# Kernel optimization log

Hardware: AMD Instinct MI355X
Metric: run time of the kernel (lower is better)

Reference implementation:

```python
import jax, jax.numpy as jnp
import numpy as np

N = 4096      # num_nodes (unbatched seq len for the transformer)
D = 128       # input_dim = window = d_model
H = 4         # num_heads
DH = D // H
DFF = 2048    # PyTorch TransformerEncoderLayer default dim_feedforward
HID = 256     # hidden_dim
OUT = 64      # output_dim
E = 131072    # num_edges (avg degree 32)
EPS = 1e-5    # LayerNorm eps (torch default)


def layer_norm(x, g, b):
    mu = jnp.mean(x, axis=-1, keepdims=True)
    var = jnp.var(x, axis=-1, keepdims=True)
    return (x - mu) * jax.lax.rsqrt(var + EPS) * g + b


def gcn_conv(x, W, b, src, dst):
    # PyG GCNConv: h = x W^T; add self-loops; symmetric deg^-1/2 norm; scatter-add at dst; + bias
    h = x @ W.T
    loop = jnp.arange(N)
    s = jnp.concatenate([src, loop])
    t = jnp.concatenate([dst, loop])
    deg = jax.ops.segment_sum(jnp.ones_like(t, dtype=h.dtype), t, num_segments=N)
    dinv = jnp.where(deg > 0, jax.lax.rsqrt(jnp.maximum(deg, 1e-12)), 0.0)
    norm = dinv[s] * dinv[t]                                   # [E+N]
    out = jax.ops.segment_sum(h[s] * norm[:, None], t, num_segments=N)
    return out + b


def setup_inputs() -> dict:
    key = jax.random.key(0)
    ks = jax.random.split(key, 12)
    sc = 0.05
    w = lambda k, shape: jax.random.normal(k, shape, dtype=jnp.float32) * sc
    return {
        "x": jax.random.normal(ks[0], (N, D), dtype=jnp.float32),
        "edge_index": jax.random.randint(ks[1], (2, E), 0, N),
        "in_proj_w": w(ks[2], (3 * D, D)),
        "in_proj_b": jnp.zeros((3 * D,), jnp.float32),
        "out_proj_w": w(ks[3], (D, D)),
        "out_proj_b": jnp.zeros((D,), jnp.float32),
        "ln1_g": jnp.ones((D,), jnp.float32),
        "ln1_b": jnp.zeros((D,), jnp.float32),
        "ffn_w1": w(ks[4], (DFF, D)),
        "ffn_b1": jnp.zeros((DFF,), jnp.float32),
        "ffn_w2": w(ks[5], (D, DFF)),
        "ffn_b2": jnp.zeros((D,), jnp.float32),
        "ln2_g": jnp.ones((D,), jnp.float32),
        "ln2_b": jnp.zeros((D,), jnp.float32),
        "gcn1_w": w(ks[6], (HID, D)),
        "gcn1_b": jnp.zeros((HID,), jnp.float32),
        "gcn2_w": w(ks[7], (HID, HID)),
        "gcn2_b": jnp.zeros((HID,), jnp.float32),
        "gcn3_w": w(ks[8], (OUT, HID)),
        "gcn3_b": jnp.zeros((OUT,), jnp.float32),
    }


def reference(x, edge_index, in_proj_w, in_proj_b, out_proj_w, out_proj_b,
              ln1_g, ln1_b, ffn_w1, ffn_b1, ffn_w2, ffn_b2, ln2_g, ln2_b,
              gcn1_w, gcn1_b, gcn2_w, gcn2_b, gcn3_w, gcn3_b):
    src, dst = edge_index[0], edge_index[1]
    # --- TransformerEncoderLayer (post-norm, relu, dropout=0, unbatched [N, D]) ---
    qkv = x @ in_proj_w.T + in_proj_b
    q, k, v = jnp.split(qkv, 3, axis=-1)
    q = q.reshape(N, H, DH)
    k = k.reshape(N, H, DH)
    v = v.reshape(N, H, DH)
    scores = jnp.einsum('nhd,mhd->hnm', q, k) / jnp.sqrt(jnp.float32(DH))
    attn = jax.nn.softmax(scores, axis=-1)
    ctx = jnp.einsum('hnm,mhd->nhd', attn, v).reshape(N, D)
    attn_out = ctx @ out_proj_w.T + out_proj_b
    y = layer_norm(x + attn_out, ln1_g, ln1_b)
    ff = jax.nn.relu(y @ ffn_w1.T + ffn_b1) @ ffn_w2.T + ffn_b2
    z = layer_norm(y + ff, ln2_g, ln2_b)
    # x.squeeze(-1) is a no-op since window (=128) > 1
    # --- 3-layer GCN with ReLU between layers ---
    h = jax.nn.relu(gcn_conv(z, gcn1_w, gcn1_b, src, dst))
    h = jax.nn.relu(gcn_conv(h, gcn2_w, gcn2_b, src, dst))
    return gcn_conv(h, gcn3_w, gcn3_b, src, dst)
```

## Files before the change

### kernel.cpp

```cpp
#include <hip/hip_runtime.h>


typedef unsigned short u16;
typedef __attribute__((ext_vector_type(8))) short bf16x8;
typedef __attribute__((ext_vector_type(4))) float f32x4;

__device__ __forceinline__ float b2f(u16 u) {
  union { unsigned int i; float f; } x; x.i = ((unsigned int)u) << 16; return x.f;
}
__device__ __forceinline__ u16 f2b(float f) {
  union { float f; unsigned int i; } x; x.f = f;
  unsigned int r = x.i + 0x7FFFu + ((x.i >> 16) & 1u);
  return (u16)(r >> 16);
}
__device__ __forceinline__ float ld1(const void* p, size_t i, int bf) {
  return bf ? b2f(((const u16*)p)[i]) : ((const float*)p)[i];
}

__device__ void gemm_body(
    int bx, int by, int bz, int nz,
    const void* __restrict__ A, const void* __restrict__ B,
    const void* __restrict__ bias, void* __restrict__ C, void* __restrict__ C2,
    int N, int K, int lda, int ldb, int bRow0, int bK0, int flags,
    const int* __restrict__ dflag, const float* __restrict__ divL)
{
  const int wbf = *dflag;
  const int abf = (flags & 64) ? 0 : ((flags & 16) ? wbf : 1);
  __shared__ u16 As[64][128];
  __shared__ u16 Bs[64][128];
  const int tid = threadIdx.x;
  const int wv = tid >> 6, l = tid & 63;
  const int lr = l & 15, lq = l >> 4;
  const int row0 = by * 64, col0 = bx * 64;
  const int qr = 32 * (wv >> 1), qc = 32 * (wv & 1);
  const int sr = tid >> 2, sb = tid & 3;
  const int Kz = K / nz;
  const int k0 = bz * Kz;
  f32x4 acc[2][2] = {};
  for (int kt = k0; kt < k0 + Kz; kt += 128) {
    __syncthreads();
#pragma unroll
    for (int g = 0; g < 4; g++) {
      int b = sb + 4 * g;
      int cc = b * 8;
      int bs = (b ^ (sr & 15)) * 8;
      size_t offA = (size_t)(row0 + sr) * lda + kt + cc;
      if (abf) {
        *(bf16x8*)&As[sr][bs] = *(const bf16x8*)((const u16*)A + offA);
      } else {
        const float* pf = (const float*)A + offA;
        float iv = divL
            ? 1.0f / divL[(size_t)((kt + cc) >> 5) * 4096 + row0 + sr]
            : 1.0f;
        float4 f0 = *(const float4*)pf, f1 = *(const float4*)(pf + 4);
        u16 t[8] = {f2b(f0.x*iv), f2b(f0.y*iv), f2b(f0.z*iv), f2b(f0.w*iv),
                    f2b(f1.x*iv), f2b(f1.y*iv), f2b(f1.z*iv), f2b(f1.w*iv)};
        *(bf16x8*)&As[sr][bs] = *(bf16x8*)t;
      }
      size_t offB = (size_t)(bRow0 + col0 + sr) * ldb + bK0 + kt + cc;
      if (wbf) {
        *(bf16x8*)&Bs[sr][bs] = *(const bf16x8*)((const u16*)B + offB);
      } else {
        const float* pf = (const float*)B + offB;
        float4 f0 = *(const float4*)pf, f1 = *(const float4*)(pf + 4);
        u16 t[8] = {f2b(f0.x), f2b(f0.y), f2b(f0.z), f2b(f0.w),
                    f2b(f1.x), f2b(f1.y), f2b(f1.z), f2b(f1.w)};
        *(bf16x8*)&Bs[sr][bs] = *(bf16x8*)t;
      }
    }
    __syncthreads();
#pragma unroll
    for (int kk = 0; kk < 4; kk++) {
      int bxs = ((4 * kk + lq) ^ lr) * 8;
      bf16x8 a0 = *(const bf16x8*)&As[qr + lr][bxs];
      bf16x8 a1 = *(const bf16x8*)&As[qr + 16 + lr][bxs];
      bf16x8 b0 = *(const bf16x8*)&Bs[qc + lr][bxs];
      bf16x8 b1 = *(const bf16x8*)&Bs[qc + 16 + lr][bxs];
      acc[0][0] = __builtin_amdgcn_mfma_f32_16x16x32_bf16(a0, b0, acc[0][0], 0, 0, 0);
      acc[0][1] = __builtin_amdgcn_mfma_f32_16x16x32_bf16(a0, b1, acc[0][1], 0, 0, 0);
      acc[1][0] = __builtin_amdgcn_mfma_f32_16x16x32_bf16(a1, b0, acc[1][0], 0, 0, 0);
      acc[1][1] = __builtin_amdgcn_mfma_f32_16x16x32_bf16(a1, b1, acc[1][1], 0, 0, 0);
    }
  }
  if ((flags & 128) && col0 >= 256) {
#pragma unroll
    for (int i = 0; i < 2; i++) {
#pragma unroll
      for (int j = 0; j < 2; j++) {
        int colg = col0 + qc + 16 * j + lr;
        int d = colg - 256;
        int rowbase = row0 + qr + 16 * i + lq * 4;
        float bb = ld1(bias, colg, wbf);
        ushort4 pv = make_ushort4(
            f2b(acc[i][j][0] + bb), f2b(acc[i][j][1] + bb),
            f2b(acc[i][j][2] + bb), f2b(acc[i][j][3] + bb));
        *(ushort4*)((u16*)C2 + (size_t)d * 4096 + rowbase) = pv;
      }
    }
    return;
  }
  const int ldc = (flags & 128) ? 256 : N;
#pragma unroll
  for (int i = 0; i < 2; i++) {
#pragma unroll
    for (int j = 0; j < 2; j++) {
#pragma unroll
      for (int r = 0; r < 4; r++) {
        int row = row0 + qr + 16 * i + lq * 4 + r;
        int col = col0 + qc + 16 * j + lr;
        float v = acc[i][j][r];
        if (flags & 8) v += ld1(bias, bRow0 + col, wbf);
        if (flags & 1) v = fmaxf(v, 0.f);
        size_t idx = (size_t)row * ldc + col;
        if (flags & 32) {
          ((float*)C)[(size_t)bz * 524288 + idx] = v;
        } else if (flags & 4) {
          float* Cf = (float*)C;
          if (flags & 2) v += Cf[idx];
          Cf[idx] = v;
        } else {
          ((u16*)C)[idx] = f2b(v);
        }
      }
    }
  }
}

__global__ __launch_bounds__(256) void gemm_mfma(
    const void* __restrict__ A, const void* __restrict__ B,
    const void* __restrict__ bias, void* __restrict__ C, void* __restrict__ C2,
    int N, int K, int lda, int ldb, int bRow0, int bK0, int flags,
    const int* __restrict__ dflag, const float* __restrict__ divL)
{
  gemm_body(blockIdx.x, blockIdx.y, blockIdx.z, gridDim.z,
            A, B, bias, C, C2, N, K, lda, ldb, bRow0, bK0, flags, dflag, divL);
}

__global__ __launch_bounds__(256) void det_zero(
    const void* __restrict__ x, int* __restrict__ flag,
    int* __restrict__ cursor)
{
  if (blockIdx.x == 0) {
    __shared__ int cnt;
    if (threadIdx.x == 0) cnt = 0;
    __syncthreads();
    const u16* p = (const u16*)x;
    int c = 0;
    for (int i = threadIdx.x; i < 4096; i += 256) {
      int e = (p[i] >> 7) & 0xFF;
      if (e >= 140) c++;
    }
    atomicAdd(&cnt, c);
    __syncthreads();
    if (threadIdx.x == 0) flag[0] = (cnt < 64) ? 1 : 0;
  } else {
    cursor[(blockIdx.x - 1) * 256 + threadIdx.x] = 0;
  }
}

__global__ __launch_bounds__(256) void csr_inproj(
    const void* __restrict__ xin, const void* __restrict__ W,
    const void* __restrict__ bias, void* __restrict__ qkQK, void* __restrict__ Vg,
    const int* __restrict__ dflag,
    const int* __restrict__ src, const int* __restrict__ dst,
    int* __restrict__ cursor, int* __restrict__ csr, int E)
{
  if (blockIdx.x < 384) {
    gemm_body(blockIdx.x % 6, blockIdx.x / 6, 0, 1,
              xin, W, bias, qkQK, Vg, 384, 128, 128, 128, 0, 0,
               8 | 16 | 128, dflag, nullptr);
  } else {
    int e = (blockIdx.x - 384) * 256 + threadIdx.x;
    if (e < E) {
      int t = dst[e];
      int pos = atomicAdd(&cursor[t], 1);
      if (pos < 128) csr[(t << 7) + pos] = src[e];
    }
  }
}

__global__ __launch_bounds__(256) void attn_part(
    const u16* __restrict__ qk, const u16* __restrict__ Vg,
    float* __restrict__ O, float* __restrict__ L)
{
  const int qt = blockIdx.x, h = blockIdx.y, kc = blockIdx.z;
  const int n0 = qt * 64;
  __shared__ u16 Qs[64][32];
  __shared__ u16 Ks[128][32];
  __shared__ u16 Vt[32][128];
  __shared__ u16 Ps[64][128];
  const int tid = threadIdx.x;
  const int wv = tid >> 6, l = tid & 63;
  const int lr = l & 15, lq = l >> 4;
  const int sr = tid >> 2, sb = tid & 3;
  const int kr = tid >> 1, kb = tid & 1;
  const int vr = tid >> 3, vb = tid & 7;
  *(bf16x8*)&Qs[sr][(sb ^ (sr & 3)) * 8] =
      *(const bf16x8*)(qk + (size_t)(n0 + sr) * 256 + h * 32 + sb * 8);
  __syncthreads();
  const float sc = 0.17677669529663687f;
  bf16x8 qf;
  {
    bf16x8 qraw = *(const bf16x8*)&Qs[16 * wv + lr][(lq ^ (lr & 3)) * 8];
#pragma unroll
    for (int t = 0; t < 8; t++)
      qf[t] = (short)f2b(b2f((u16)qraw[t]) * sc);
  }
  f32x4 o0 = {}, o1 = {};
  float psum[4] = {0.f, 0.f, 0.f, 0.f};
  for (int t = 0; t < 8; t++) {
    const int m0 = kc * 1024 + t * 128;
    __syncthreads();
#pragma unroll
    for (int cc = 0; cc < 2; cc++) {
      int ch = kb + 2 * cc;
      *(bf16x8*)&Ks[kr][(ch ^ (kr & 3)) * 8] =
          *(const bf16x8*)(qk + (size_t)(m0 + kr) * 256 + 128 + h * 32 + ch * 8);
    }
#pragma unroll
    for (int cc = 0; cc < 2; cc++) {
      int ch = vb + 8 * cc;
      *(bf16x8*)&Vt[vr][(ch ^ (vr & 15)) * 8] =
          *(const bf16x8*)(Vg + (size_t)(h * 32 + vr) * 4096 + m0 + ch * 8);
    }
    __syncthreads();
    f32x4 s[8];
#pragma unroll
    for (int jt = 0; jt < 8; jt++) {
      bf16x8 kf = *(const bf16x8*)&Ks[16 * jt + lr][(lq ^ (lr & 3)) * 8];
      f32x4 z = {};
      s[jt] = __builtin_amdgcn_mfma_f32_16x16x32_bf16(qf, kf, z, 0, 0, 0);
    }
#pragma unroll
    for (int jt = 0; jt < 8; jt++)
#pragma unroll
      for (int r = 0; r < 4; r++) {
        float p = __expf(s[jt][r]);
        psum[r] += p;
        int qrow = 16 * wv + lq * 4 + r;
        int ch = 2 * jt + (lr >> 3);
        Ps[qrow][(ch ^ (qrow & 15)) * 8 + (lr & 7)] = f2b(p);
      }
    __syncthreads();
#pragma unroll
    for (int kk = 0; kk < 4; kk++) {
      int prow = 16 * wv + lr;
      bf16x8 pf = *(const bf16x8*)&Ps[prow][((4 * kk + lq) ^ (lr & 15)) * 8];
      bf16x8 v0 = *(const bf16x8*)&Vt[lr][((4 * kk + lq) ^ (lr & 15)) * 8];
      bf16x8 v1 = *(const bf16x8*)&Vt[16 + lr][((4 * kk + lq) ^ (lr & 15)) * 8];
      o0 = __builtin_amdgcn_mfma_f32_16x16x32_bf16(pf, v0, o0, 0, 0, 0);
      o1 = __builtin_amdgcn_mfma_f32_16x16x32_bf16(pf, v1, o1, 0, 0, 0);
    }
  }
  const size_t ko = (size_t)kc * 524288;
  float* Lk = L + (size_t)kc * 16384;
#pragma unroll
  for (int r = 0; r < 4; r++) {
    int row = n0 + 16 * wv + lq * 4 + r;
    O[ko + (size_t)row * 128 + h * 32 + lr]      = o0[r];
    O[ko + (size_t)row * 128 + h * 32 + 16 + lr] = o1[r];
    float ps = psum[r];
    ps += __shfl_xor(ps, 1); ps += __shfl_xor(ps, 2);
    ps += __shfl_xor(ps, 4); ps += __shfl_xor(ps, 8);
    if (lr == 0) Lk[h * 4096 + row] = ps;
  }
}

__global__ __launch_bounds__(256) void oproj_ln(
    const float* __restrict__ Op, const float* __restrict__ Lp,
    const void* __restrict__ W, const void* __restrict__ bias,
    const void* __restrict__ x, const void* __restrict__ g,
    const void* __restrict__ bln, u16* __restrict__ y_bf,
    float* __restrict__ y_f32, const int* __restrict__ dflag)
{
  const int wbf = *dflag;
  __shared__ u16 As[16][128];
  __shared__ u16 Bs[128][128];
  const int tid = threadIdx.x;
  const int r0 = blockIdx.x * 16;
  {
    int r = tid >> 4, b = tid & 15;
    int hh = b >> 2;
    float Ls = Lp[hh * 4096 + r0 + r] + Lp[16384 + hh * 4096 + r0 + r]
             + Lp[32768 + hh * 4096 + r0 + r] + Lp[49152 + hh * 4096 + r0 + r];
    float iv = 1.0f / Ls;
    float a8[8] = {};
#pragma unroll
    for (int kc = 0; kc < 4; kc++) {
      const float* p = Op + (size_t)kc * 524288 + (size_t)(r0 + r) * 128 + b * 8;
      float4 q0 = *(const float4*)p, q1 = *(const float4*)(p + 4);
      a8[0] += q0.x; a8[1] += q0.y; a8[2] += q0.z; a8[3] += q0.w;
      a8[4] += q1.x; a8[5] += q1.y; a8[6] += q1.z; a8[7] += q1.w;
    }
    u16 t[8];
#pragma unroll
    for (int j = 0; j < 8; j++) t[j] = f2b(a8[j] * iv);
    *(bf16x8*)&As[r][(b ^ r) * 8] = *(bf16x8*)t;
  }
  {
    int o = tid >> 1, half = tid & 1;
#pragma unroll
    for (int bb8 = 0; bb8 < 8; bb8++) {
      int b = half * 8 + bb8;
      size_t off = (size_t)o * 128 + b * 8;
      if (wbf) {
        *(bf16x8*)&Bs[o][(b ^ (o & 15)) * 8] = *(const bf16x8*)((const u16*)W + off);
      } else {
        const float* pf = (const float*)W + off;
        float4 f0 = *(const float4*)pf, f1 = *(const float4*)(pf + 4);
        u16 t[8] = {f2b(f0.x), f2b(f0.y), f2b(f0.z), f2b(f0.w),
                    f2b(f1.x), f2b(f1.y), f2b(f1.z), f2b(f1.w)};
        *(bf16x8*)&Bs[o][(b ^ (o & 15)) * 8] = *(bf16x8*)t;
      }
    }
  }
  __syncthreads();
  const int wv = tid >> 6, l = tid & 63;
  const int lr = l & 15, lq = l >> 4;
  const int c0 = 32 * wv;
  f32x4 acc[2] = {};
#pragma unroll
  for (int kk = 0; kk < 4; kk++) {
    int bxs = ((4 * kk + lq) ^ lr) * 8;
    bf16x8 a0 = *(const bf16x8*)&As[lr][bxs];
    bf16x8 b0 = *(const bf16x8*)&Bs[c0 + lr][bxs];
    bf16x8 b1 = *(const bf16x8*)&Bs[c0 + 16 + lr][bxs];
    acc[0] = __builtin_amdgcn_mfma_f32_16x16x32_bf16(a0, b0, acc[0], 0, 0, 0);
    acc[1] = __builtin_amdgcn_mfma_f32_16x16x32_bf16(a0, b1, acc[1], 0, 0, 0);
  }
  __syncthreads();
  float* Cf = (float*)&Bs[0][0];
#pragma unroll
  for (int j = 0; j < 2; j++)
#pragma unroll
    for (int r = 0; r < 4; r++) {
      int row = lq * 4 + r, col = c0 + 16 * j + lr;
      float v = acc[j][r] + ld1(bias, col, wbf)
              + ld1(x, (size_t)(r0 + row) * 128 + col, wbf);
      Cf[row * 128 + col] = v;
    }
  __syncthreads();
#pragma unroll
  for (int it = 0; it < 4; it++) {
    int row = it * 4 + wv;
    float v0 = Cf[row * 128 + l], v1 = Cf[row * 128 + 64 + l];
    float s = v0 + v1, sq = v0 * v0 + v1 * v1;
    for (int off = 32; off; off >>= 1) { s += __shfl_down(s, off); sq += __shfl_down(sq, off); }
    s = __shfl(s, 0); sq = __shfl(sq, 0);
    float mu = s * (1.f / 128.f);
    float var = sq * (1.f / 128.f) - mu * mu;
    float rs = rsqrtf(var + 1e-5f);
    float o0 = (v0 - mu) * rs * ld1(g, l, wbf) + ld1(bln, l, wbf);
    float o1 = (v1 - mu) * rs * ld1(g, l + 64, wbf) + ld1(bln, l + 64, wbf);
    size_t i0 = (size_t)(r0 + row) * 128 + l;
    y_bf[i0] = f2b(o0); y_bf[i0 + 64] = f2b(o1);
    y_f32[i0] = o0; y_f32[i0 + 64] = o1;
  }
}

__global__ __launch_bounds__(256) void ln_res(
    const void* __restrict__ A, int a_mode, const float* __restrict__ R,
    int nacc, const void* __restrict__ rbias,
    const void* __restrict__ g, const void* __restrict__ b,
    u16* __restrict__ out_bf, float* __restrict__ out_f32,
    const int* __restrict__ dflag)
{
  const int wbf = *dflag;
  const int abf = a_mode ? wbf : 0;
  int row = blockIdx.x * 4 + (threadIdx.x >> 6);
  int lane = threadIdx.x & 63;
  size_t i0 = (size_t)row * 128 + lane, i1 = i0 + 64;
  float r0a = 0.f, r1a = 0.f;
  for (int z = 0; z < nacc; z++) {
    r0a += R[(size_t)z * 524288 + i0];
    r1a += R[(size_t)z * 524288 + i1];
  }
  float v0 = ld1(A, i0, abf) + r0a;
  float v1 = ld1(A, i1, abf) + r1a;
  if (rbias) { v0 += ld1(rbias, lane, wbf); v1 += ld1(rbias, lane + 64, wbf); }
  float s = v0 + v1, sq = v0 * v0 + v1 * v1;
  for (int off = 32; off; off >>= 1) { s += __shfl_down(s, off); sq += __shfl_down(sq, off); }
  s = __shfl(s, 0); sq = __shfl(sq, 0);
  float mu = s * (1.f / 128.f);
  float var = sq * (1.f / 128.f) - mu * mu;
  float rs = rsqrtf(var + 1e-5f);
  float r0 = (v0 - mu) * rs * ld1(g, lane, wbf) + ld1(b, lane, wbf);
  float r1 = (v1 - mu) * rs * ld1(g, lane + 64, wbf) + ld1(b, lane + 64, wbf);
  out_bf[i0] = f2b(r0);
  out_bf[i1] = f2b(r1);
  if (out_f32) { out_f32[i0] = r0; out_f32[i1] = r1; }
}

__global__ __launch_bounds__(256) void gcn_gather8(
    const u16* __restrict__ h, const int* __restrict__ deg,
    const int* __restrict__ csr, u16* __restrict__ out, int F)
{
  const int ft = F >> 3;
  const int tpn = ft << 1;
  const int node = blockIdx.x * (256 / tpn) + threadIdx.x / tpn;
  const int wl = threadIdx.x & 63;
  const int gl = threadIdx.x % tpn;
  const int sub = gl / ft;
  const int f = (gl % ft) * 8;
  const int gbase = wl - gl;
  int dn = deg[node]; if (dn > 128) dn = 128;
  float di = rsqrtf((float)(dn + 1));
  float a[8] = {};
  if (sub == 0) {
    bf16x8 hv = *(const bf16x8*)(h + (size_t)node * F + f);
#pragma unroll
    for (int j = 0; j < 8; j++) a[j] = di * b2f((u16)hv[j]);
  }
  const int e0 = node << 7;
  for (int base = 0; base < dn; base += tpn) {
    int lim = dn - base; if (lim > tpn) lim = tpn;
    int mi = 0;
    if (gl < lim) mi = csr[e0 + base + gl];
    float mds = rsqrtf((float)(deg[mi] + 1));
    int nj = (lim - sub + 1) >> 1;
    int njmax = (lim + 1) >> 1;
    for (int jj = 0; jj < njmax; jj += 2) {
      int sA = __shfl(mi, gbase + 2 * jj + sub);
      float dA = __shfl(mds, gbase + 2 * jj + sub);
      int sB = __shfl(mi, gbase + 2 * jj + 2 + sub);
      float dB = __shfl(mds, gbase + 2 * jj + 2 + sub);
      bool pA = (jj < nj), pB = (jj + 1 < nj);
      bf16x8 svA, svB;
      if (pA) svA = *(const bf16x8*)(h + (size_t)sA * F + f);
      if (pB) svB = *(const bf16x8*)(h + (size_t)sB * F + f);
      if (pA) {
#pragma unroll
        for (int j = 0; j < 8; j++) a[j] += dA * b2f((u16)svA[j]);
      }
      if (pB) {
#pragma unroll
        for (int j = 0; j < 8; j++) a[j] += dB * b2f((u16)svB[j]);
      }
    }
  }
#pragma unroll
  for (int j = 0; j < 8; j++) a[j] += __shfl_xor(a[j], ft);
  if (sub) return;
  u16 t[8];
#pragma unroll
  for (int j = 0; j < 8; j++) t[j] = f2b(a[j] * di);
  *(bf16x8*)(out + (size_t)node * F + f) = *(bf16x8*)t;
}

__global__ __launch_bounds__(256) void gcn_gather(
    const u16* __restrict__ h, const int* __restrict__ deg,
    const int* __restrict__ csr,
    const void* __restrict__ bias, void* __restrict__ out,
    int F, const int* __restrict__ dflag)
{
  const int wbf = *dflag;
  const int tpn = F >> 2;
  const int node = blockIdx.x * (256 / tpn) + threadIdx.x / tpn;
  const int wl = threadIdx.x & 63;
  const int gl = threadIdx.x % tpn;
  const int f = gl * 4;
  const int gbase = wl - gl;
  int dn = deg[node]; if (dn > 128) dn = 128;
  float di = rsqrtf((float)(dn + 1));
  ushort4 hv = *(const ushort4*)(h + (size_t)node * F + f);
  float a0 = di * b2f(hv.x), a1 = di * b2f(hv.y);
  float a2 = di * b2f(hv.z), a3 = di * b2f(hv.w);
  const int e0 = node << 7;
  for (int base = 0; base < dn; base += tpn) {
    int lim = dn - base; if (lim > tpn) lim = tpn;
    int mi = 0;
    if (gl < lim) mi = csr[e0 + base + gl];
    float mds = rsqrtf((float)(deg[mi] + 1));
    for (int j = 0; j < lim; j += 2) {
      int s0 = __shfl(mi, gbase + j);
      float d0 = __shfl(mds, gbase + j);
      int s1 = __shfl(mi, gbase + j + 1);
      float d1 = __shfl(mds, gbase + j + 1);
      bool p1 = (j + 1 < lim);
      ushort4 sv0 = *(const ushort4*)(h + (size_t)s0 * F + f);
      ushort4 sv1;
      if (p1) sv1 = *(const ushort4*)(h + (size_t)s1 * F + f);
      a0 += d0 * b2f(sv0.x); a1 += d0 * b2f(sv0.y);
      a2 += d0 * b2f(sv0.z); a3 += d0 * b2f(sv0.w);
      if (p1) {
        a0 += d1 * b2f(sv1.x); a1 += d1 * b2f(sv1.y);
        a2 += d1 * b2f(sv1.z); a3 += d1 * b2f(sv1.w);
      }
    }
  }
  float b0 = bias ? ld1(bias, f, wbf)     : 0.f;
  float b1 = bias ? ld1(bias, f + 1, wbf) : 0.f;
  float b2 = bias ? ld1(bias, f + 2, wbf) : 0.f;
  float b3 = bias ? ld1(bias, f + 3, wbf) : 0.f;
  float v0 = a0 * di + b0, v1 = a1 * di + b1;
  float v2 = a2 * di + b2, v3 = a3 * di + b3;
  size_t idx = (size_t)node * F + f;
  if (wbf) {
    *(ushort4*)((u16*)out + idx) = make_ushort4(f2b(v0), f2b(v1), f2b(v2), f2b(v3));
  } else {
    *(float4*)((float*)out + idx) = make_float4(v0, v1, v2, v3);
  }
}

extern "C" void kernel_launch(void* const* d_in, const int* in_sizes, int n_in,
                              void* d_out, int out_size, void* d_ws, size_t ws_size,
                              hipStream_t stream)
{
  const void* x          = d_in[0];
  const int*  edge       = (const int*)d_in[1];
  const void* in_proj_w  = d_in[2];
  const void* in_proj_b  = d_in[3];
  const void* out_proj_w = d_in[4];
  const void* out_proj_b = d_in[5];
  const void* ln1_g      = d_in[6];
  const void* ln1_b      = d_in[7];
  const void* ffn_w1     = d_in[8];
  const void* ffn_b1     = d_in[9];
  const void* ffn_w2     = d_in[10];
  const void* ffn_b2     = d_in[11];
  const void* ln2_g      = d_in[12];
  const void* ln2_b      = d_in[13];
  const void* g1w        = d_in[14];
  const void* g1b        = d_in[15];
  const void* g2w        = d_in[16];
  const void* g2b        = d_in[17];
  const void* g3w        = d_in[18];
  const void* g3b        = d_in[19];
  const int E = in_sizes[1] / 2;
  const int* esrc = edge;
  const int* edst = edge + E;

  char* wsb     = (char*)d_ws;
  u16*   qkQK   = (u16*)(wsb + 0);
  u16*   Vg     = (u16*)(wsb + 2097152);
  float* Op     = (float*)(wsb + 3145728);
  float* Lp     = (float*)(wsb + 11534336);
  int*   cursor = (int*)(wsb + 11796480);
  int*   dflag  = (int*)(wsb + 11812864);
  int*   csr    = (int*)(wsb + 11829248);
  float* y_f32  = (float*)(wsb + 13926400);
  u16*   y_bf   = (u16*)(wsb + 16023552);
  u16*   z_bf   = (u16*)(wsb + 17072128);
  u16*   az     = (u16*)(wsb + 18120704);
  u16*   h1     = (u16*)(wsb + 19169280);
  u16*   ah1    = (u16*)(wsb + 21266432);
  u16*   h2     = (u16*)(wsb + 23363584);
  u16*   t3     = (u16*)(wsb + 25460736);
  u16*   ff1    = (u16*)(wsb + 25985024);
  float* ff2p   = (float*)(wsb + 42762240);

  det_zero<<<17, 256, 0, stream>>>(x, dflag, cursor);
  csr_inproj<<<896, 256, 0, stream>>>(x, in_proj_w, in_proj_b, qkQK, Vg, dflag,
      esrc, edst, cursor, csr, E);

  attn_part<<<dim3(64, 4, 4), 256, 0, stream>>>(qkQK, Vg, Op, Lp);
  oproj_ln<<<256, 256, 0, stream>>>(Op, Lp, out_proj_w, out_proj_b, x,
      ln1_g, ln1_b, y_bf, y_f32, dflag);
  gemm_mfma<<<dim3(32, 64), 256, 0, stream>>>(y_bf, ffn_w1, ffn_b1, ff1, nullptr,
      2048, 128, 128, 128, 0, 0,  1 | 8, dflag, nullptr);
  gemm_mfma<<<dim3(2, 64, 4), 256, 0, stream>>>(ff1, ffn_w2, nullptr, ff2p, nullptr,
      128, 2048, 2048, 2048, 0, 0,  32, dflag, nullptr);
  ln_res<<<1024, 256, 0, stream>>>(y_f32, 0, ff2p, 4, ffn_b2, ln2_g, ln2_b,
      z_bf, nullptr, dflag);

  gcn_gather8<<<512, 256, 0, stream>>>(z_bf, cursor, csr, az, 128);
  gemm_mfma<<<dim3(4, 64), 256, 0, stream>>>(az, g1w, g1b, h1, nullptr,
      256, 128, 128, 128, 0, 0,  1 | 8, dflag, nullptr);
  gcn_gather8<<<1024, 256, 0, stream>>>(h1, cursor, csr, ah1, 256);
  gemm_mfma<<<dim3(4, 64), 256, 0, stream>>>(ah1, g2w, g2b, h2, nullptr,
      256, 256, 256, 256, 0, 0,  1 | 8, dflag, nullptr);
  gemm_mfma<<<dim3(1, 64), 256, 0, stream>>>(h2, g3w, nullptr, t3, nullptr,
      64, 256, 256, 256, 0, 0, 0, dflag, nullptr);
  gcn_gather<<<256, 256, 0, stream>>>(t3, cursor, csr, g3b, d_out, 64, dflag);
}
```

Measured before the change: 246.8 us.

## Fuse FFN2 split-K GEMM with residual LayerNorm via last-block reduction; unroll gathers

Merges the FFN second GEMM and the residual LayerNorm into one kernel. The last split-K block for each 64-row tile, found with an atomic counter, sums the partial results and applies the LayerNorm, which removes one kernel launch and its dependency gap. Separately, the GCN gather loops are unrolled to issue four neighbor loads per iteration instead of two, giving more memory-level parallelism. The cost is atomics and threadfences, extra serial LayerNorm work in the last block of each tile, and a done-counter array that must be reset.

New measurement: 321.6 us. 1.3x slower.

```diff
diff --git a/kernel.cpp b/kernel.cpp
--- a/kernel.cpp
+++ b/kernel.cpp
@@ -136,9 +136,58 @@
             A, B, bias, C, C2, N, K, lda, ldb, bRow0, bK0, flags, dflag, divL);
 }
 
+__global__ __launch_bounds__(256) void gemm_w2ln(
+    const void* __restrict__ A, const void* __restrict__ B,
+    void* __restrict__ C,
+    const float* __restrict__ yf, const void* __restrict__ rbias,
+    const void* __restrict__ g, const void* __restrict__ bln,
+    u16* __restrict__ out_bf, int* __restrict__ done,
+    const int* __restrict__ dflag)
+{
+  gemm_body(blockIdx.x, blockIdx.y, blockIdx.z, gridDim.z,
+            A, B, nullptr, C, nullptr, 128, 2048, 2048, 2048, 0, 0,
+             32, dflag, nullptr);
+  __threadfence();
+  __shared__ int lastf;
+  if (threadIdx.x == 0)
+    lastf = (atomicAdd(&done[blockIdx.y], 1) == 7);
+  __syncthreads();
+  if (!lastf) return;
+  __threadfence();
+  const int wbf = *dflag;
+  const float* R = (const float*)C;
+  const int lane = threadIdx.x & 63;
+  for (int rr = threadIdx.x >> 6; rr < 64; rr += 4) {
+    int row = blockIdx.y * 64 + rr;
+    size_t i0 = (size_t)row * 128 + lane, i1 = i0 + 64;
+    float r0a = 0.f, r1a = 0.f;
+#pragma unroll
+    for (int z = 0; z < 4; z++) {
+      r0a += R[(size_t)z * 524288 + i0];
+      r1a += R[(size_t)z * 524288 + i1];
+    }
+    float v0 = yf[i0] + r0a;
+    float v1 = yf[i1] + r1a;
+    v0 += ld1(rbias, lane, wbf); v1 += ld1(rbias, lane + 64, wbf);
+    float s = v0 + v1, sq = v0 * v0 + v1 * v1;
+    for (int off = 32; off; off >>= 1) { s += __shfl_down(s, off); sq += __shfl_down(sq, off); }
+    s = __shfl(s, 0); sq = __shfl(sq, 0);
+    float mu = s * (1.f / 128.f);
+    float var = sq * (1.f / 128.f) - mu * mu;
+    float rs = rsqrtf(var + 1e-5f);
+    float o0 = (v0 - mu) * rs * ld1(g, lane, wbf) + ld1(bln, lane, wbf);
+    float o1 = (v1 - mu) * rs * ld1(g, lane + 64, wbf) + ld1(bln, lane + 64, wbf);
+    out_bf[i0] = f2b(o0);
+    out_bf[i1] = f2b(o1);
+  }
+  __threadfence();
+  __syncthreads();
+  if (threadIdx.x == 0) done[blockIdx.y] = 0;
+}
+
 __global__ __launch_bounds__(256) void det_zero(
     const void* __restrict__ x, int* __restrict__ flag,
-    int* __restrict__ cursor)
+    int* __restrict__ cursor, int* __restrict__ done)
 {
   if (blockIdx.x == 0) {
     __shared__ int cnt;
@@ -151,6 +200,7 @@
       if (e >= 140) c++;
     }
     atomicAdd(&cnt, c);
+    if (threadIdx.x < 64) done[threadIdx.x] = 0;
     __syncthreads();
     if (threadIdx.x == 0) flag[0] = (cnt < 64) ? 1 : 0;
   } else {
@@ -358,39 +408,6 @@
   }
 }
 
-__global__ __launch_bounds__(256) void ln_res(
-    const void* __restrict__ A, int a_mode, const float* __restrict__ R,
-    int nacc, const void* __restrict__ rbias,
-    const void* __restrict__ g, const void* __restrict__ b,
-    u16* __restrict__ out_bf, float* __restrict__ out_f32,
-    const int* __restrict__ dflag)
-{
-  const int wbf = *dflag;
-  const int abf = a_mode ? wbf : 0;
-  int row = blockIdx.x * 4 + (threadIdx.x >> 6);
-  int lane = threadIdx.x & 63;
-  size_t i0 = (size_t)row * 128 + lane, i1 = i0 + 64;
-  float r0a = 0.f, r1a = 0.f;
-  for (int z = 0; z < nacc; z++) {
-    r0a += R[(size_t)z * 524288 + i0];
-    r1a += R[(size_t)z * 524288 + i1];
-  }
-  float v0 = ld1(A, i0, abf) + r0a;
-  float v1 = ld1(A, i1, abf) + r1a;
-  if (rbias) { v0 += ld1(rbias, lane, wbf); v1 += ld1(rbias, lane + 64, wbf); }
-  float s = v0 + v1, sq = v0 * v0 + v1 * v1;
-  for (int off = 32; off; off >>= 1) { s += __shfl_down(s, off); sq += __shfl_down(sq, off); }
-  s = __shfl(s, 0); sq = __shfl(sq, 0);
-  float mu = s * (1.f / 128.f);
-  float var = sq * (1.f / 128.f) - mu * mu;
-  float rs = rsqrtf(var + 1e-5f);
-  float r0 = (v0 - mu) * rs * ld1(g, lane, wbf) + ld1(b, lane, wbf);
-  float r1 = (v1 - mu) * rs * ld1(g, lane + 64, wbf) + ld1(b, lane + 64, wbf);
-  out_bf[i0] = f2b(r0);
-  out_bf[i1] = f2b(r1);
-  if (out_f32) { out_f32[i0] = r0; out_f32[i1] = r1; }
-}
-
 __global__ __launch_bounds__(256) void gcn_gather8(
     const u16* __restrict__ h, const int* __restrict__ deg,
     const int* __restrict__ csr, u16* __restrict__ out, int F)
@@ -419,15 +436,22 @@
     float mds = rsqrtf((float)(deg[mi] + 1));
     int nj = (lim - sub + 1) >> 1;
     int njmax = (lim + 1) >> 1;
-    for (int jj = 0; jj < njmax; jj += 2) {
+    for (int jj = 0; jj < njmax; jj += 4) {
       int sA = __shfl(mi, gbase + 2 * jj + sub);
       float dA = __shfl(mds, gbase + 2 * jj + sub);
       int sB = __shfl(mi, gbase + 2 * jj + 2 + sub);
       float dB = __shfl(mds, gbase + 2 * jj + 2 + sub);
+      int sC = __shfl(mi, gbase + 2 * jj + 4 + sub);
+      float dC = __shfl(mds, gbase + 2 * jj + 4 + sub);
+      int sD = __shfl(mi, gbase + 2 * jj + 6 + sub);
+      float dD = __shfl(mds, gbase + 2 * jj + 6 + sub);
       bool pA = (jj < nj), pB = (jj + 1 < nj);
-      bf16x8 svA, svB;
+      bool pC = (jj + 2 < nj), pD = (jj + 3 < nj);
+      bf16x8 svA, svB, svC, svD;
       if (pA) svA = *(const bf16x8*)(h + (size_t)sA * F + f);
       if (pB) svB = *(const bf16x8*)(h + (size_t)sB * F + f);
+      if (pC) svC = *(const bf16x8*)(h + (size_t)sC * F + f);
+      if (pD) svD = *(const bf16x8*)(h + (size_t)sD * F + f);
       if (pA) {
 #pragma unroll
         for (int j = 0; j < 8; j++) a[j] += dA * b2f((u16)svA[j]);
@@ -435,6 +459,14 @@
       if (pB) {
 #pragma unroll
         for (int j = 0; j < 8; j++) a[j] += dB * b2f((u16)svB[j]);
+      }
+      if (pC) {
+#pragma unroll
+        for (int j = 0; j < 8; j++) a[j] += dC * b2f((u16)svC[j]);
+      }
+      if (pD) {
+#pragma unroll
+        for (int j = 0; j < 8; j++) a[j] += dD * b2f((u16)svD[j]);
       }
     }
   }
@@ -471,20 +503,34 @@
     int mi = 0;
     if (gl < lim) mi = csr[e0 + base + gl];
     float mds = rsqrtf((float)(deg[mi] + 1));
-    for (int j = 0; j < lim; j += 2) {
+    for (int j = 0; j < lim; j += 4) {
       int s0 = __shfl(mi, gbase + j);
       float d0 = __shfl(mds, gbase + j);
       int s1 = __shfl(mi, gbase + j + 1);
       float d1 = __shfl(mds, gbase + j + 1);
-      bool p1 = (j + 1 < lim);
+      int s2 = __shfl(mi, gbase + j + 2);
+      float d2 = __shfl(mds, gbase + j + 2);
+      int s3 = __shfl(mi, gbase + j + 3);
+      float d3 = __shfl(mds, gbase + j + 3);
+      bool p1 = (j + 1 < lim), p2 = (j + 2 < lim), p3 = (j + 3 < lim);
       ushort4 sv0 = *(const ushort4*)(h + (size_t)s0 * F + f);
-      ushort4 sv1;
+      ushort4 sv1, sv2, sv3;
       if (p1) sv1 = *(const ushort4*)(h + (size_t)s1 * F + f);
+      if (p2) sv2 = *(const ushort4*)(h + (size_t)s2 * F + f);
+      if (p3) sv3 = *(const ushort4*)(h + (size_t)s3 * F + f);
       a0 += d0 * b2f(sv0.x); a1 += d0 * b2f(sv0.y);
       a2 += d0 * b2f(sv0.z); a3 += d0 * b2f(sv0.w);
       if (p1) {
         a0 += d1 * b2f(sv1.x); a1 += d1 * b2f(sv1.y);
         a2 += d1 * b2f(sv1.z); a3 += d1 * b2f(sv1.w);
+      }
+      if (p2) {
+        a0 += d2 * b2f(sv2.x); a1 += d2 * b2f(sv2.y);
+        a2 += d2 * b2f(sv2.z); a3 += d2 * b2f(sv2.w);
+      }
+      if (p3) {
+        a0 += d3 * b2f(sv3.x); a1 += d3 * b2f(sv3.y);
+        a2 += d3 * b2f(sv3.z); a3 += d3 * b2f(sv3.w);
       }
     }
   }
@@ -537,6 +583,7 @@
   float* Lp     = (float*)(wsb + 11534336);
   int*   cursor = (int*)(wsb + 11796480);
   int*   dflag  = (int*)(wsb + 11812864);
+  int*   done   = (int*)(wsb + 11813888);
   int*   csr    = (int*)(wsb + 11829248);
   float* y_f32  = (float*)(wsb + 13926400);
   u16*   y_bf   = (u16*)(wsb + 16023552);
@@ -549,7 +596,7 @@
   u16*   ff1    = (u16*)(wsb + 25985024);
   float* ff2p   = (float*)(wsb + 42762240);
 
-  det_zero<<<17, 256, 0, stream>>>(x, dflag, cursor);
+  det_zero<<<17, 256, 0, stream>>>(x, dflag, cursor, done);
   csr_inproj<<<896, 256, 0, stream>>>(x, in_proj_w, in_proj_b, qkQK, Vg, dflag,
       esrc, edst, cursor, csr, E);
 
@@ -558,10 +605,8 @@
       ln1_g, ln1_b, y_bf, y_f32, dflag);
   gemm_mfma<<<dim3(32, 64), 256, 0, stream>>>(y_bf, ffn_w1, ffn_b1, ff1, nullptr,
       2048, 128, 128, 128, 0, 0,  1 | 8, dflag, nullptr);
-  gemm_mfma<<<dim3(2, 64, 4), 256, 0, stream>>>(ff1, ffn_w2, nullptr, ff2p, nullptr,
-      128, 2048, 2048, 2048, 0, 0,  32, dflag, nullptr);
-  ln_res<<<1024, 256, 0, stream>>>(y_f32, 0, ff2p, 4, ffn_b2, ln2_g, ln2_b,
-      z_bf, nullptr, dflag);
+  gemm_w2ln<<<dim3(2, 64, 4), 256, 0, stream>>>(ff1, ffn_w2, ff2p,
+      y_f32, ffn_b2, ln2_g, ln2_b, z_bf, done, dflag);
 
   gcn_gather8<<<512, 256, 0, stream>>>(z_bf, cursor, csr, az, 128);
   gemm_mfma<<<dim3(4, 64), 256, 0, stream>>>(az, g1w, g1b, h1, nullptr,
```
